# Kernel tuning notes

Measured on AMD Instinct MI355X. Metric: run time of the kernel, lower is better.

The kernel has to match this reference:

```python
import jax, jax.numpy as jnp
import numpy as np

D_MODEL = 1024
N_INPUT = 4096
N_PROCESS = 2048
D_ROUTING = 256
TEMPERATURE = 0.5
LN_EPS = 1e-5


def _gelu(x):
    return jax.nn.gelu(x, approximate=False)  # torch F.gelu default (erf)


def setup_inputs() -> dict:
    key = jax.random.key(0)
    ks = jax.random.split(key, 10)
    B, S = 8, 2048
    x = jax.random.normal(ks[0], (B, S, D_MODEL), dtype=jnp.float32)
    # GlobalRouter query_net: Linear(d_model, 2*d_routing) -> GELU -> LayerNorm -> Linear(2*d_routing, d_routing)
    W1 = jax.random.normal(ks[1], (2 * D_ROUTING, D_MODEL), dtype=jnp.float32) * (2.0 / (D_MODEL + 2 * D_ROUTING)) ** 0.5 * 1.414
    b1 = jnp.zeros((2 * D_ROUTING,), dtype=jnp.float32)
    ln_g = jnp.ones((2 * D_ROUTING,), dtype=jnp.float32)
    ln_b = jnp.zeros((2 * D_ROUTING,), dtype=jnp.float32)
    W2 = jax.random.normal(ks[2], (D_ROUTING, 2 * D_ROUTING), dtype=jnp.float32) * (2.0 / (3 * D_ROUTING)) ** 0.5 * 1.414
    b2 = jnp.zeros((D_ROUTING,), dtype=jnp.float32)
    neuron_keys = jax.random.normal(ks[3], (N_INPUT, D_ROUTING), dtype=jnp.float32) / D_ROUTING ** 0.5 * 1.414
    input_patterns = jax.random.normal(ks[4], (N_INPUT, D_MODEL), dtype=jnp.float32) / D_MODEL ** 0.5 * 1.414
    process_weights = jax.random.normal(ks[5], (N_PROCESS, N_INPUT), dtype=jnp.float32) / N_INPUT ** 0.5 * 1.414
    process_outputs = jax.random.normal(ks[6], (N_PROCESS, D_MODEL), dtype=jnp.float32) / D_MODEL ** 0.5 * 1.414
    return {
        'x': x, 'k_input': 2048, 'k_process': 1024,
        'W1': W1, 'b1': b1, 'ln_g': ln_g, 'ln_b': ln_b, 'W2': W2, 'b2': b2,
        'neuron_keys': neuron_keys, 'input_patterns': input_patterns,
        'process_weights': process_weights, 'process_outputs': process_outputs,
    }


def _forward(x, k_input, k_process, W1, b1, ln_g, ln_b, W2, b2,
             neuron_keys, input_patterns, process_weights, process_outputs):
    B, S, d_model = x.shape
    # ---- GlobalRouter ----
    gctx = jnp.max(x, axis=1)                                  # [B, d_model]
    h = _gelu(gctx @ W1.T + b1)                                # [B, 2*d_routing]
    mu = jnp.mean(h, axis=-1, keepdims=True)
    var = jnp.mean((h - mu) ** 2, axis=-1, keepdims=True)
    h = (h - mu) * jax.lax.rsqrt(var + LN_EPS) * ln_g + ln_b
    query = h @ W2.T + b2                                      # [B, d_routing]
    logits = (query @ neuron_keys.T) / D_ROUTING ** 0.5        # [B, n_input]
    probs = jax.nn.softmax(logits / TEMPERATURE, axis=-1)
    _, input_idx = jax.lax.top_k(logits, k_input)              # [B, k_input]
    one_hot = jnp.zeros_like(probs).at[jnp.arange(B)[:, None], input_idx].set(1.0)
    routing_weights = jax.lax.stop_gradient(one_hot - probs) + probs  # STE
    # ---- input neuron stage ----
    input_acts = _gelu(jnp.einsum('bsd,nd->bsn', x, input_patterns))   # [B,S,n_input]
    weighted = input_acts * routing_weights[:, None, :]
    sel_in = jnp.take_along_axis(weighted, input_idx[:, None, :], axis=2)  # [B,S,k_input]
    # gather process weight columns per batch: [B, n_process, k_input]
    W_sel = jnp.transpose(process_weights[:, input_idx], (1, 0, 2))
    process_acts = _gelu(jnp.einsum('bsk,bpk->bsp', sel_in, W_sel))    # [B,S,n_process]
    # ---- process neuron stage ----
    process_scores = jnp.mean(process_acts, axis=1)                    # [B,n_process]
    _, process_idx = jax.lax.top_k(process_scores, k_process)          # [B,k_process]
    sel_proc = jnp.take_along_axis(process_acts, process_idx[:, None, :], axis=2)  # [B,S,k_process]
    out_sel = process_outputs[process_idx]                             # [B,k_process,d_model]
    return jnp.einsum('bsp,bpd->bsd', sel_proc, out_sel)


def reference(x, k_input, k_process, W1, b1, ln_g, ln_b, W2, b2,
              neuron_keys, input_patterns, process_weights, process_outputs):
    return _forward(x, k_input, k_process, W1, b1, ln_g, ln_b, W2, b2,
                    neuron_keys, input_patterns, process_weights, process_outputs)
```

## Files before the change

### kernel.cpp

```cpp
#include <hip/hip_runtime.h>
#include <stdint.h>

#define B_  8
#define S_  2048
#define DM  1024
#define NI  4096
#define NP  2048
#define DR  256
#define H2  512
#define KI  2048
#define KP  1024
#define LDW 40

typedef __attribute__((ext_vector_type(8))) short bf16x8;
typedef __attribute__((ext_vector_type(4))) float f32x4;
typedef unsigned short ushort;
typedef unsigned int uint;

__device__ __forceinline__ float gelu_erf(float v){
    return 0.5f * v * (1.0f + erff(v * 0.7071067811865476f));
}
__device__ __forceinline__ ushort f2b(float f){
    union { float f; uint u; } a; a.f = f;
    uint r = a.u + 0x7fffu + ((a.u >> 16) & 1u);
    return (ushort)(r >> 16);
}
__device__ __forceinline__ float b2f(ushort u){
    union { uint u; float f; } a; a.u = ((uint)u) << 16; return a.f;
}
__device__ __forceinline__ void cvt8(const float* p, uint4& H, uint4& L){
    uint h[4], l[4];
    #pragma unroll
    for(int i = 0; i < 4; i++){
        ushort h0 = f2b(p[2*i]);   float f0 = b2f(h0); ushort l0 = f2b(p[2*i]   - f0);
        ushort h1 = f2b(p[2*i+1]); float f1 = b2f(h1); ushort l1 = f2b(p[2*i+1] - f1);
        h[i] = (uint)h0 | ((uint)h1 << 16);
        l[i] = (uint)l0 | ((uint)l1 << 16);
    }
    H = uint4{h[0],h[1],h[2],h[3]};
    L = uint4{l[0],l[1],l[2],l[3]};
}

__global__ __launch_bounds__(256) void k_gpart(const float* __restrict__ x,
                                               float* __restrict__ gpart){
    int b = blockIdx.x >> 4, ch = blockIdx.x & 15;
    const float4* xb = (const float4*)(x + ((size_t)b*S_ + (size_t)ch*128) * DM);
    int t = threadIdx.x;
    float4 m = xb[t];
    for(int r = 1; r < 128; r++){
        float4 v = xb[(size_t)r*(DM/4) + t];
        m.x = fmaxf(m.x, v.x); m.y = fmaxf(m.y, v.y);
        m.z = fmaxf(m.z, v.z); m.w = fmaxf(m.w, v.w);
    }
    ((float4*)(gpart + (size_t)(b*16 + ch)*DM))[t] = m;
}

__global__ __launch_bounds__(256) void k_h(const float* __restrict__ gpart,
                                           const float* __restrict__ W1,
                                           const float* __restrict__ b1,
                                           float* __restrict__ h){
    __shared__ float g[DM];
    int b = blockIdx.x >> 3, ig = blockIdx.x & 7;
    int t = threadIdx.x;
    for(int d = t; d < DM; d += 256){
        float m = gpart[(size_t)(b*16)*DM + d];
        for(int c = 1; c < 16; c++) m = fmaxf(m, gpart[(size_t)(b*16 + c)*DM + d]);
        g[d] = m;
    }
    __syncthreads();
    int i  = ig*64 + (t >> 2);
    int dq = (t & 3) * 256;
    const float* wr = W1 + (size_t)i*DM + dq;
    const float* gg = g + dq;
    float s = 0.f;
    for(int d = 0; d < 256; d++) s = fmaf(gg[d], wr[d], s);
    s += __shfl_xor(s, 1);
    s += __shfl_xor(s, 2);
    if((t & 3) == 0) h[b*H2 + i] = gelu_erf(s + b1[i]);
}

__global__ __launch_bounds__(256) void k_query(const float* __restrict__ h,
                                               const float* __restrict__ lng,
                                               const float* __restrict__ lnb,
                                               const float* __restrict__ W2,
                                               const float* __restrict__ b2,
                                               float* __restrict__ query){
    __shared__ float hn[H2];
    __shared__ float red[4];
    int b = blockIdx.x >> 2, qg = blockIdx.x & 3;
    int t = threadIdx.x;
    float v0 = h[b*H2 + t], v1 = h[b*H2 + 256 + t];
    float s = v0 + v1;
    for(int o = 32; o > 0; o >>= 1) s += __shfl_down(s, o);
    if((t & 63) == 0) red[t >> 6] = s;
    __syncthreads();
    float mean = (red[0] + red[1] + red[2] + red[3]) * (1.f/H2);
    __syncthreads();
    float d0 = v0 - mean, d1 = v1 - mean;
    float sq = d0*d0 + d1*d1;
    for(int o = 32; o > 0; o >>= 1) sq += __shfl_down(sq, o);
    if((t & 63) == 0) red[t >> 6] = sq;
    __syncthreads();
    float var  = (red[0] + red[1] + red[2] + red[3]) * (1.f/H2);
    float rstd = rsqrtf(var + 1e-5f);
    hn[t]       = d0*rstd*lng[t]       + lnb[t];
    hn[256 + t] = d1*rstd*lng[256 + t] + lnb[256 + t];
    __syncthreads();
    int q  = qg*64 + (t >> 2);
    int iq = (t & 3) * 128;
    const float* wr = W2 + (size_t)q*H2 + iq;
    float acc = 0.f;
    for(int i2 = 0; i2 < 128; i2++) acc = fmaf(hn[iq + i2], wr[i2], acc);
    acc += __shfl_xor(acc, 1);
    acc += __shfl_xor(acc, 2);
    if((t & 3) == 0) query[b*DR + q] = acc + b2[q];
}

__global__ __launch_bounds__(256) void k_logits(const float* __restrict__ query,
                                                const float* __restrict__ nk,
                                                float* __restrict__ logits){
    __shared__ float q[DR];
    int b = blockIdx.x >> 4, ng = blockIdx.x & 15;
    int t = threadIdx.x;
    if(t < DR) q[t] = query[b*DR + t];
    __syncthreads();
    int n = ng*256 + t;
    const float* kr = nk + (size_t)n*DR;
    float s = 0.f;
    for(int i = 0; i < DR; i++) s = fmaf(q[i], kr[i], s);
    logits[b*NI + n] = s * 0.0625f;
}

template<int N_, int KSEL>
__global__ __launch_bounds__(256) void k_topk(const float* __restrict__ vals,
                                              int* __restrict__ idxout){
    __shared__ unsigned u[N_];
    __shared__ int redc[4];
    __shared__ int sc[256];
    int t = threadIdx.x;
    size_t vbase = (size_t)blockIdx.x * N_;
    size_t obase = (size_t)blockIdx.x * KSEL;
    for(int i = t; i < N_; i += 256){
        unsigned bits = __float_as_uint(vals[vbase + i]);
        u[i] = (bits & 0x80000000u) ? ~bits : (bits | 0x80000000u);
    }
    __syncthreads();
    unsigned lo = 0u, hi = 0xFFFFFFFFu;
    while(lo < hi){
        unsigned mid = lo + (unsigned)((((unsigned long long)(hi - lo)) + 1ull) >> 1);
        int c = 0;
        for(int i = t; i < N_; i += 256) c += (u[i] >= mid) ? 1 : 0;
        for(int o = 32; o > 0; o >>= 1) c += __shfl_down(c, o);
        if((t & 63) == 0) redc[t >> 6] = c;
        __syncthreads();
        int tot = redc[0] + redc[1] + redc[2] + redc[3];
        if(tot >= KSEL) lo = mid; else hi = mid - 1;
        __syncthreads();
    }
    unsigned T = lo;
    const int PER = N_ / 256;
    int base = t * PER;
    int lgt = 0, leq = 0;
    for(int j = 0; j < PER; j++){
        unsigned v = u[base + j];
        lgt += (v > T) ? 1 : 0; leq += (v == T) ? 1 : 0;
    }
    sc[t] = (lgt << 16) | leq;
    __syncthreads();
    for(int o = 1; o < 256; o <<= 1){
        int add = (t >= o) ? sc[t - o] : 0;
        __syncthreads();
        sc[t] += add;
        __syncthreads();
    }
    int need = KSEL - (sc[255] >> 16);
    int ex = (t == 0) ? 0 : sc[t - 1];
    int pos = (ex >> 16) + ((ex & 0xffff) < need ? (ex & 0xffff) : need);
    int eq = ex & 0xffff;
    for(int j = 0; j < PER; j++){
        unsigned v = u[base + j];
        if(v > T){ idxout[obase + pos++] = base + j; }
        else if(v == T){ if(eq < need){ idxout[obase + pos++] = base + j; } eq++; }
    }
}

__global__ __launch_bounds__(256) void k_gemm1(const float* __restrict__ x,
                                               const float* __restrict__ patt,
                                               const int* __restrict__ iidx,
                                               ushort* __restrict__ selh,
                                               ushort* __restrict__ sell, int b0){
    __shared__ __align__(16) ushort Ah[128*LDW], Al[128*LDW], Bh[128*LDW], Bl[128*LDW];
    __shared__ int rowmap[128];
    int t = threadIdx.x;
    int g = blockIdx.x >> 8, rest = blockIdx.x & 255;
    int b = b0 + g;
    int mb = rest >> 4, nb = rest & 15;
    int m0 = mb*128, n0 = nb*128;
    ushort* selh_g = selh + (size_t)g*S_*KI;
    ushort* sell_g = sell + (size_t)g*S_*KI;
    if(t < 128) rowmap[t] = iidx[(size_t)b*KI + n0 + t];
    __syncthreads();
    int r = t & 127, half = t >> 7;
    const float* ag = x    + (size_t)b*S_*DM + (size_t)(m0 + r)*DM + half*16;
    const float* bg = patt + (size_t)rowmap[r]*DM + half*16;
    float4 fa[4], fb[4];
    #pragma unroll
    for(int i = 0; i < 4; i++){ fa[i] = *(const float4*)(ag + i*4); fb[i] = *(const float4*)(bg + i*4); }
    int w = t >> 6, lane = t & 63;
    int mbase = (w >> 1)*64, nbase = (w & 1)*64;
    int lm = lane & 15, q = lane >> 4;
    f32x4 acc[4][4];
    #pragma unroll
    for(int i = 0; i < 4; i++)
      #pragma unroll
      for(int j = 0; j < 4; j++) acc[i][j] = f32x4{0.f,0.f,0.f,0.f};
    for(int k0 = 0; k0 < DM; k0 += 32){
        uint4 AH0, AL0, AH1, AL1, BH0, BL0, BH1, BL1;
        cvt8((const float*)&fa[0], AH0, AL0); cvt8((const float*)&fa[2], AH1, AL1);
        cvt8((const float*)&fb[0], BH0, BL0); cvt8((const float*)&fb[2], BH1, BL1);
        __syncthreads();
        *(uint4*)(Ah + r*LDW + half*16)     = AH0;
        *(uint4*)(Ah + r*LDW + half*16 + 8) = AH1;
        *(uint4*)(Al + r*LDW + half*16)     = AL0;
        *(uint4*)(Al + r*LDW + half*16 + 8) = AL1;
        *(uint4*)(Bh + r*LDW + half*16)     = BH0;
        *(uint4*)(Bh + r*LDW + half*16 + 8) = BH1;
        *(uint4*)(Bl + r*LDW + half*16)     = BL0;
        *(uint4*)(Bl + r*LDW + half*16 + 8) = BL1;
        __syncthreads();
        if(k0 + 32 < DM){
            ag += 32; bg += 32;
            #pragma unroll
            for(int i = 0; i < 4; i++){ fa[i] = *(const float4*)(ag + i*4); fb[i] = *(const float4*)(bg + i*4); }
        }
        bf16x8 ahf[4], alf[4];
        #pragma unroll
        for(int mt = 0; mt < 4; mt++){
            ahf[mt] = *(const bf16x8*)(Ah + (mbase + mt*16 + lm)*LDW + q*8);
            alf[mt] = *(const bf16x8*)(Al + (mbase + mt*16 + lm)*LDW + q*8);
        }
        #pragma unroll
        for(int nt = 0; nt < 4; nt++){
            bf16x8 bhf = *(const bf16x8*)(Bh + (nbase + nt*16 + lm)*LDW + q*8);
            bf16x8 blf = *(const bf16x8*)(Bl + (nbase + nt*16 + lm)*LDW + q*8);
            #pragma unroll
            for(int mt = 0; mt < 4; mt++){
                acc[mt][nt] = __builtin_amdgcn_mfma_f32_16x16x32_bf16(ahf[mt], bhf, acc[mt][nt], 0, 0, 0);
                acc[mt][nt] = __builtin_amdgcn_mfma_f32_16x16x32_bf16(ahf[mt], blf, acc[mt][nt], 0, 0, 0);
                acc[mt][nt] = __builtin_amdgcn_mfma_f32_16x16x32_bf16(alf[mt], bhf, acc[mt][nt], 0, 0, 0);
            }
        }
    }
    #pragma unroll
    for(int mt = 0; mt < 4; mt++)
      #pragma unroll
      for(int nt = 0; nt < 4; nt++){
        int col = n0 + nbase + nt*16 + lm;
        #pragma unroll
        for(int i = 0; i < 4; i++){
            int row = m0 + mbase + mt*16 + q*4 + i;
            float gv = gelu_erf(acc[mt][nt][i]);
            ushort hbits = f2b(gv);
            selh_g[(size_t)row*KI + col] = hbits;
            sell_g[(size_t)row*KI + col] = f2b(gv - b2f(hbits));
        }
      }
}

__global__ __launch_bounds__(256) void k_gather_wsel(const float* __restrict__ pw,
                                                     const int* __restrict__ iidx,
                                                     ushort* __restrict__ wh,
                                                     ushort* __restrict__ wl,
                                                     float* __restrict__ scores, int b0){
    __shared__ int kidx[KI];
    int g = blockIdx.x >> 8, pc = blockIdx.x & 255;
    int b = b0 + g;
    ushort* wh_g = wh + (size_t)g*NP*KI;
    ushort* wl_g = wl + (size_t)g*NP*KI;
    int t = threadIdx.x;
    for(int i = t; i < KI; i += 256) kidx[i] = iidx[(size_t)b*KI + i];
    if(t < 8) scores[(size_t)b*NP + pc*8 + t] = 0.f;
    __syncthreads();
    for(int r2 = 0; r2 < 8; r2++){
        int p = pc*8 + r2;
        const float* row = pw + (size_t)p*NI;
        for(int j = t; j < KI; j += 256){
            float v = row[kidx[j]];
            ushort hb = f2b(v);
            wh_g[(size_t)p*KI + j] = hb;
            wl_g[(size_t)p*KI + j] = f2b(v - b2f(hb));
        }
    }
}

__global__ __launch_bounds__(256) void k_gemm2(const ushort* __restrict__ selh,
                                               const ushort* __restrict__ sell,
                                               const ushort* __restrict__ wh,
                                               const ushort* __restrict__ wl,
                                               ushort* __restrict__ acts,
                                               float* __restrict__ scores, int b0){
    __shared__ __align__(16) ushort Ah[128*LDW], Al[128*LDW], Bh[128*LDW], Bl[128*LDW];
    __shared__ float colsum[128];
    int t = threadIdx.x;
    int g = blockIdx.x >> 8, rest = blockIdx.x & 255;
    int b = b0 + g;
    int mb = rest >> 4, nb = rest & 15;
    int m0 = mb*128, n0 = nb*128;
    const ushort* selh_g = selh + (size_t)g*S_*KI;
    const ushort* sell_g = sell + (size_t)g*S_*KI;
    const ushort* wh_g   = wh   + (size_t)g*NP*KI;
    const ushort* wl_g   = wl   + (size_t)g*NP*KI;
    ushort* acts_g = acts + (size_t)g*S_*NP;
    int r = t & 127, half = t >> 7;
    const ushort* ahg = selh_g + (size_t)(m0 + r)*KI + half*16;
    const ushort* alg = sell_g + (size_t)(m0 + r)*KI + half*16;
    const ushort* bhg = wh_g   + (size_t)(n0 + r)*KI + half*16;
    const ushort* blg = wl_g   + (size_t)(n0 + r)*KI + half*16;
    uint4 AH0, AH1, AL0, AL1, BH0, BH1, BL0, BL1;
    AH0 = *(const uint4*)(ahg); AH1 = *(const uint4*)(ahg + 8);
    AL0 = *(const uint4*)(alg); AL1 = *(const uint4*)(alg + 8);
    BH0 = *(const uint4*)(bhg); BH1 = *(const uint4*)(bhg + 8);
    BL0 = *(const uint4*)(blg); BL1 = *(const uint4*)(blg + 8);
    int w = t >> 6, lane = t & 63;
    int mbase = (w >> 1)*64, nbase = (w & 1)*64;
    int lm = lane & 15, q = lane >> 4;
    f32x4 acc[4][4];
    #pragma unroll
    for(int i = 0; i < 4; i++)
      #pragma unroll
      for(int j = 0; j < 4; j++) acc[i][j] = f32x4{0.f,0.f,0.f,0.f};
    for(int k0 = 0; k0 < KI; k0 += 32){
        __syncthreads();
        *(uint4*)(Ah + r*LDW + half*16)     = AH0;
        *(uint4*)(Ah + r*LDW + half*16 + 8) = AH1;
        *(uint4*)(Al + r*LDW + half*16)     = AL0;
        *(uint4*)(Al + r*LDW + half*16 + 8) = AL1;
        *(uint4*)(Bh + r*LDW + half*16)     = BH0;
        *(uint4*)(Bh + r*LDW + half*16 + 8) = BH1;
        *(uint4*)(Bl + r*LDW + half*16)     = BL0;
        *(uint4*)(Bl + r*LDW + half*16 + 8) = BL1;
        __syncthreads();
        if(k0 + 32 < KI){
            ahg += 32; alg += 32; bhg += 32; blg += 32;
            AH0 = *(const uint4*)(ahg); AH1 = *(const uint4*)(ahg + 8);
            AL0 = *(const uint4*)(alg); AL1 = *(const uint4*)(alg + 8);
            BH0 = *(const uint4*)(bhg); BH1 = *(const uint4*)(bhg + 8);
            BL0 = *(const uint4*)(blg); BL1 = *(const uint4*)(blg + 8);
        }
        bf16x8 ahf[4], alf[4];
        #pragma unroll
        for(int mt = 0; mt < 4; mt++){
            ahf[mt] = *(const bf16x8*)(Ah + (mbase + mt*16 + lm)*LDW + q*8);
            alf[mt] = *(const bf16x8*)(Al + (mbase + mt*16 + lm)*LDW + q*8);
        }
        #pragma unroll
        for(int nt = 0; nt < 4; nt++){
            bf16x8 bhf = *(const bf16x8*)(Bh + (nbase + nt*16 + lm)*LDW + q*8);
            bf16x8 blf = *(const bf16x8*)(Bl + (nbase + nt*16 + lm)*LDW + q*8);
            #pragma unroll
            for(int mt = 0; mt < 4; mt++){
                acc[mt][nt] = __builtin_amdgcn_mfma_f32_16x16x32_bf16(ahf[mt], bhf, acc[mt][nt], 0, 0, 0);
                acc[mt][nt] = __builtin_amdgcn_mfma_f32_16x16x32_bf16(ahf[mt], blf, acc[mt][nt], 0, 0, 0);
                acc[mt][nt] = __builtin_amdgcn_mfma_f32_16x16x32_bf16(alf[mt], bhf, acc[mt][nt], 0, 0, 0);
            }
        }
    }
    if(t < 128) colsum[t] = 0.f;
    __syncthreads();
    #pragma unroll
    for(int mt = 0; mt < 4; mt++)
      #pragma unroll
      for(int nt = 0; nt < 4; nt++){
        int cb = nbase + nt*16 + lm;
        float s4 = 0.f;
        #pragma unroll
        for(int i = 0; i < 4; i++){
            int row = m0 + mbase + mt*16 + q*4 + i;
            float gv = gelu_erf(acc[mt][nt][i]);
            s4 += gv;
            acts_g[(size_t)row*NP + n0 + cb] = f2b(gv);
        }
        atomicAdd(&colsum[cb], s4);
      }
    __syncthreads();
    if(t < 128) atomicAdd(&scores[(size_t)b*NP + n0 + t], colsum[t]);
}

__global__ __launch_bounds__(256) void k_gather_selacts(const ushort* __restrict__ acts,
                                                        const int* __restrict__ pidx,
                                                        ushort* __restrict__ selacts, int b0){
    __shared__ int pix[KP];
    int g = blockIdx.x >> 6, sc_ = blockIdx.x & 63;
    int b = b0 + g;
    const ushort* acts_g = acts + (size_t)g*S_*NP;
    ushort* selacts_g = selacts + (size_t)g*S_*KP;
    int t = threadIdx.x;
    for(int i = t; i < KP; i += 256) pix[i] = pidx[(size_t)b*KP + i];
    __syncthreads();
    const ushort* Ab = acts_g    + ((size_t)sc_*32)*NP;
    ushort*       Ob = selacts_g + ((size_t)sc_*32)*KP;
    for(int r2 = 0; r2 < 32; r2++){
        for(int j = t; j < KP; j += 256)
            Ob[(size_t)r2*KP + j] = Ab[(size_t)r2*NP + pix[j]];
    }
}

__global__ __launch_bounds__(256) void k_gemm3(const ushort* __restrict__ selacts,
                                               const float* __restrict__ pout,
                                               const int* __restrict__ pidx,
                                               float* __restrict__ out, int b0){
    __shared__ __align__(16) ushort As[128*LDW], Bs[128*LDW];
    __shared__ int pix[KP];
    int t = threadIdx.x;
    int g = blockIdx.x >> 7, rest = blockIdx.x & 127;
    int b = b0 + g;
    int mb = rest >> 3, nb = rest & 7;
    int m0 = mb*128, n0 = nb*128;
    const ushort* selacts_g = selacts + (size_t)g*S_*KP;
    for(int i = t; i < KP; i += 256) pix[i] = pidx[(size_t)b*KP + i];
    __syncthreads();
    int r = t & 127, half = t >> 7;
    const ushort* ag = selacts_g + (size_t)(m0 + r)*KP + half*16;
    int kk = t >> 3, nc = (t & 7)*16;
    uint4 A0 = *(const uint4*)(ag), A1 = *(const uint4*)(ag + 8);
    float4 fb[4];
    {
        const float* bg = pout + (size_t)pix[kk]*DM + n0 + nc;
        #pragma unroll
        for(int i = 0; i < 4; i++) fb[i] = *(const float4*)(bg + i*4);
    }
    int w = t >> 6, lane = t & 63;
    int mbase = (w >> 1)*64, nbase = (w & 1)*64;
    int lm = lane & 15, q = lane >> 4;
    f32x4 acc[4][4];
    #pragma unroll
    for(int i = 0; i < 4; i++)
      #pragma unroll
      for(int j = 0; j < 4; j++) acc[i][j] = f32x4{0.f,0.f,0.f,0.f};
    for(int k0 = 0; k0 < KP; k0 += 32){
        __syncthreads();
        *(uint4*)(As + r*LDW + half*16)     = A0;
        *(uint4*)(As + r*LDW + half*16 + 8) = A1;
        {
            const float* pf = (const float*)fb;
            #pragma unroll
            for(int c = 0; c < 16; c++) Bs[(nc + c)*LDW + kk] = f2b(pf[c]);
        }
        __syncthreads();
        if(k0 + 32 < KP){
            ag += 32;
            A0 = *(const uint4*)(ag); A1 = *(const uint4*)(ag + 8);
            const float* bg = pout + (size_t)pix[k0 + 32 + kk]*DM + n0 + nc;
            #pragma unroll
            for(int i = 0; i < 4; i++) fb[i] = *(const float4*)(bg + i*4);
        }
        bf16x8 af[4];
        #pragma unroll
        for(int mt = 0; mt < 4; mt++)
            af[mt] = *(const bf16x8*)(As + (mbase + mt*16 + lm)*LDW + q*8);
        #pragma unroll
        for(int nt = 0; nt < 4; nt++){
            bf16x8 bf = *(const bf16x8*)(Bs + (nbase + nt*16 + lm)*LDW + q*8);
            #pragma unroll
            for(int mt = 0; mt < 4; mt++)
                acc[mt][nt] = __builtin_amdgcn_mfma_f32_16x16x32_bf16(af[mt], bf, acc[mt][nt], 0, 0, 0);
        }
    }
    float* Cb = out + (size_t)b*S_*DM;
    #pragma unroll
    for(int mt = 0; mt < 4; mt++)
      #pragma unroll
      for(int nt = 0; nt < 4; nt++){
        int col = n0 + nbase + nt*16 + lm;
        #pragma unroll
        for(int i = 0; i < 4; i++){
            int row = m0 + mbase + mt*16 + q*4 + i;
            Cb[(size_t)row*DM + col] = acc[mt][nt][i];
        }
      }
}

extern "C" void kernel_launch(void* const* d_in, const int* in_sizes, int n_in,
                              void* d_out, int out_size, void* d_ws, size_t ws_size,
                              hipStream_t stream){
    const float* x    = (const float*)d_in[0];
    const float* W1   = (const float*)d_in[3];
    const float* b1   = (const float*)d_in[4];
    const float* lng  = (const float*)d_in[5];
    const float* lnb  = (const float*)d_in[6];
    const float* W2   = (const float*)d_in[7];
    const float* b2   = (const float*)d_in[8];
    const float* nk   = (const float*)d_in[9];
    const float* patt = (const float*)d_in[10];
    const float* pw   = (const float*)d_in[11];
    const float* pout = (const float*)d_in[12];
    float* out = (float*)d_out;

    const size_t fixed =
        ((size_t)B_*16*DM*4 + 255 & ~(size_t)255) + ((size_t)B_*H2*4 + 255 & ~(size_t)255) +
        ((size_t)B_*DR*4 + 255 & ~(size_t)255)    + ((size_t)B_*NI*4 + 255 & ~(size_t)255) +
        ((size_t)B_*KI*4 + 255 & ~(size_t)255)    + ((size_t)B_*NP*4 + 255 & ~(size_t)255) +
        ((size_t)B_*KP*4 + 255 & ~(size_t)255);
    const size_t perb = (size_t)S_*KI*2*2 + (size_t)NP*KI*2*2 + (size_t)S_*NP*2 + (size_t)S_*KP*2 + 6*256;
    int G = 4;
    while(G > 1 && fixed + (size_t)G*perb > ws_size) G >>= 1;
    if(fixed + (size_t)G*perb > ws_size) return;

    char* wsp = (char*)d_ws;
    size_t off = 0;
    auto alloc = [&](size_t bytes) -> void* {
        void* p = wsp + off;
        off += (bytes + 255) & ~(size_t)255;
        return p;
    };
    float*  gpart   = (float*) alloc((size_t)B_*16*DM*4);
    float*  h       = (float*) alloc((size_t)B_*H2*4);
    float*  query   = (float*) alloc((size_t)B_*DR*4);
    float*  logits  = (float*) alloc((size_t)B_*NI*4);
    int*    iidx    = (int*)   alloc((size_t)B_*KI*4);
    float*  scores  = (float*) alloc((size_t)B_*NP*4);
    int*    pidx    = (int*)   alloc((size_t)B_*KP*4);
    ushort* selh    = (ushort*)alloc((size_t)G*S_*KI*2);
    ushort* sell    = (ushort*)alloc((size_t)G*S_*KI*2);
    ushort* wselh   = (ushort*)alloc((size_t)G*NP*KI*2);
    ushort* wsell   = (ushort*)alloc((size_t)G*NP*KI*2);
    ushort* acts    = (ushort*)alloc((size_t)G*S_*NP*2);
    ushort* selacts = (ushort*)alloc((size_t)G*S_*KP*2);

    dim3 blk(256);
    k_gpart <<<128, blk, 0, stream>>>(x, gpart);
    k_h     <<<64,  blk, 0, stream>>>(gpart, W1, b1, h);
    k_query <<<32,  blk, 0, stream>>>(h, lng, lnb, W2, b2, query);
    k_logits<<<128, blk, 0, stream>>>(query, nk, logits);
    k_topk<NI, KI><<<B_, blk, 0, stream>>>(logits, iidx);
    for(int b0 = 0; b0 < B_; b0 += G){
        k_gemm1        <<<G*256, blk, 0, stream>>>(x, patt, iidx, selh, sell, b0);
        k_gather_wsel  <<<G*256, blk, 0, stream>>>(pw, iidx, wselh, wsell, scores, b0);
        k_gemm2        <<<G*256, blk, 0, stream>>>(selh, sell, wselh, wsell, acts, scores, b0);
        k_topk<NP, KP> <<<G,     blk, 0, stream>>>(scores + (size_t)b0*NP, pidx + (size_t)b0*KP);
        k_gather_selacts<<<G*64, blk, 0, stream>>>(acts, pidx, selacts, b0);
        k_gemm3        <<<G*128, blk, 0, stream>>>(selacts, pout, pidx, out, b0);
    }
}
```

Before: 1.512 ms.

## Use fp16 MFMA for gemm1/gemm3 with pre-converted inputs and swizzled LDS

```diff
diff --git a/kernel.cpp b/kernel.cpp
--- a/kernel.cpp
+++ b/kernel.cpp
@@ -13,6 +13,7 @@
 #define LDW 40
 
 typedef __attribute__((ext_vector_type(8))) short bf16x8;
+typedef __attribute__((ext_vector_type(8))) _Float16 f16x8;
 typedef __attribute__((ext_vector_type(4))) float f32x4;
 typedef unsigned short ushort;
 typedef unsigned int uint;
@@ -28,17 +29,23 @@
 __device__ __forceinline__ float b2f(ushort u){
     union { uint u; float f; } a; a.u = ((uint)u) << 16; return a.f;
 }
-__device__ __forceinline__ void cvt8(const float* p, uint4& H, uint4& L){
-    uint h[4], l[4];
-    #pragma unroll
-    for(int i = 0; i < 4; i++){
-        ushort h0 = f2b(p[2*i]);   float f0 = b2f(h0); ushort l0 = f2b(p[2*i]   - f0);
-        ushort h1 = f2b(p[2*i+1]); float f1 = b2f(h1); ushort l1 = f2b(p[2*i+1] - f1);
-        h[i] = (uint)h0 | ((uint)h1 << 16);
-        l[i] = (uint)l0 | ((uint)l1 << 16);
-    }
-    H = uint4{h[0],h[1],h[2],h[3]};
-    L = uint4{l[0],l[1],l[2],l[3]};
+__device__ __forceinline__ ushort f2h(float f){
+    union { _Float16 h; ushort u; } v; v.h = (_Float16)f; return v.u;
+}
+
+#define SWZ_ST(r, c)  ((r)*32 + ((((c) ^ (((r) >> 1) & 3))) << 3))
+
+__global__ __launch_bounds__(256) void k_cvt(const float* __restrict__ in,
+                                             ushort* __restrict__ out, int n8){
+    int i = blockIdx.x*256 + threadIdx.x;
+    int stride = gridDim.x*256;
+    for(; i < n8; i += stride){
+        const float* p = in + (size_t)i*8;
+        ushort h[8];
+        #pragma unroll
+        for(int j = 0; j < 8; j++) h[j] = f2h(p[j]);
+        *(uint4*)(out + (size_t)i*8) = *(uint4*)h;
+    }
 }
 
 __global__ __launch_bounds__(256) void k_gpart(const float* __restrict__ x,
@@ -184,12 +191,12 @@
     }
 }
 
-__global__ __launch_bounds__(256) void k_gemm1(const float* __restrict__ x,
-                                               const float* __restrict__ patt,
+__global__ __launch_bounds__(256) void k_gemm1(const ushort* __restrict__ x16,
+                                               const ushort* __restrict__ patt16,
                                                const int* __restrict__ iidx,
                                                ushort* __restrict__ selh,
                                                ushort* __restrict__ sell, int b0){
-    __shared__ __align__(16) ushort Ah[128*LDW], Al[128*LDW], Bh[128*LDW], Bl[128*LDW];
+    __shared__ __align__(16) ushort As[128*32], Bs[128*32];
     __shared__ int rowmap[128];
     int t = threadIdx.x;
     int g = blockIdx.x >> 8, rest = blockIdx.x & 255;
@@ -200,56 +207,46 @@
     ushort* sell_g = sell + (size_t)g*S_*KI;
     if(t < 128) rowmap[t] = iidx[(size_t)b*KI + n0 + t];
     __syncthreads();
-    int r = t & 127, half = t >> 7;
-    const float* ag = x    + (size_t)b*S_*DM + (size_t)(m0 + r)*DM + half*16;
-    const float* bg = patt + (size_t)rowmap[r]*DM + half*16;
-    float4 fa[4], fb[4];
-    #pragma unroll
-    for(int i = 0; i < 4; i++){ fa[i] = *(const float4*)(ag + i*4); fb[i] = *(const float4*)(bg + i*4); }
+    int c = t & 3, r2 = t >> 2;
+    const ushort* a0p = x16 + (size_t)b*S_*DM + (size_t)(m0 + r2)*DM + c*8;
+    const ushort* a1p = a0p + (size_t)64*DM;
+    const ushort* b0p = patt16 + (size_t)rowmap[r2]*DM + c*8;
+    const ushort* b1p = patt16 + (size_t)rowmap[r2 + 64]*DM + c*8;
+    uint4 A0 = *(const uint4*)a0p, A1 = *(const uint4*)a1p;
+    uint4 B0 = *(const uint4*)b0p, B1 = *(const uint4*)b1p;
+    int st0 = SWZ_ST(r2, c);
+    int st1 = st0 + 64*32;
     int w = t >> 6, lane = t & 63;
     int mbase = (w >> 1)*64, nbase = (w & 1)*64;
     int lm = lane & 15, q = lane >> 4;
+    int fq = ((q ^ ((lm >> 1) & 3)) << 3);
     f32x4 acc[4][4];
     #pragma unroll
     for(int i = 0; i < 4; i++)
       #pragma unroll
       for(int j = 0; j < 4; j++) acc[i][j] = f32x4{0.f,0.f,0.f,0.f};
     for(int k0 = 0; k0 < DM; k0 += 32){
-        uint4 AH0, AL0, AH1, AL1, BH0, BL0, BH1, BL1;
-        cvt8((const float*)&fa[0], AH0, AL0); cvt8((const float*)&fa[2], AH1, AL1);
-        cvt8((const float*)&fb[0], BH0, BL0); cvt8((const float*)&fb[2], BH1, BL1);
-        __syncthreads();
-        *(uint4*)(Ah + r*LDW + half*16)     = AH0;
-        *(uint4*)(Ah + r*LDW + half*16 + 8) = AH1;
-        *(uint4*)(Al + r*LDW + half*16)     = AL0;
-        *(uint4*)(Al + r*LDW + half*16 + 8) = AL1;
-        *(uint4*)(Bh + r*LDW + half*16)     = BH0;
-        *(uint4*)(Bh + r*LDW + half*16 + 8) = BH1;
-        *(uint4*)(Bl + r*LDW + half*16)     = BL0;
-        *(uint4*)(Bl + r*LDW + half*16 + 8) = BL1;
+        __syncthreads();
+        *(uint4*)(As + st0) = A0; *(uint4*)(As + st1) = A1;
+        *(uint4*)(Bs + st0) = B0; *(uint4*)(Bs + st1) = B1;
         __syncthreads();
         if(k0 + 32 < DM){
-            ag += 32; bg += 32;
-            #pragma unroll
-            for(int i = 0; i < 4; i++){ fa[i] = *(const float4*)(ag + i*4); fb[i] = *(const float4*)(bg + i*4); }
-        }
-        bf16x8 ahf[4], alf[4];
-        #pragma unroll
-        for(int mt = 0; mt < 4; mt++){
-            ahf[mt] = *(const bf16x8*)(Ah + (mbase + mt*16 + lm)*LDW + q*8);
-            alf[mt] = *(const bf16x8*)(Al + (mbase + mt*16 + lm)*LDW + q*8);
-        }
-        #pragma unroll
-        for(int nt = 0; nt < 4; nt++){
-            bf16x8 bhf = *(const bf16x8*)(Bh + (nbase + nt*16 + lm)*LDW + q*8);
-            bf16x8 blf = *(const bf16x8*)(Bl + (nbase + nt*16 + lm)*LDW + q*8);
-            #pragma unroll
-            for(int mt = 0; mt < 4; mt++){
-                acc[mt][nt] = __builtin_amdgcn_mfma_f32_16x16x32_bf16(ahf[mt], bhf, acc[mt][nt], 0, 0, 0);
-                acc[mt][nt] = __builtin_amdgcn_mfma_f32_16x16x32_bf16(ahf[mt], blf, acc[mt][nt], 0, 0, 0);
-                acc[mt][nt] = __builtin_amdgcn_mfma_f32_16x16x32_bf16(alf[mt], bhf, acc[mt][nt], 0, 0, 0);
-            }
-        }
+            a0p += 32; a1p += 32; b0p += 32; b1p += 32;
+            A0 = *(const uint4*)a0p; A1 = *(const uint4*)a1p;
+            B0 = *(const uint4*)b0p; B1 = *(const uint4*)b1p;
+        }
+        f16x8 af[4], bf[4];
+        #pragma unroll
+        for(int mt = 0; mt < 4; mt++)
+            af[mt] = *(const f16x8*)(As + (mbase + mt*16 + lm)*32 + fq);
+        #pragma unroll
+        for(int nt = 0; nt < 4; nt++)
+            bf[nt] = *(const f16x8*)(Bs + (nbase + nt*16 + lm)*32 + fq);
+        #pragma unroll
+        for(int nt = 0; nt < 4; nt++)
+          #pragma unroll
+          for(int mt = 0; mt < 4; mt++)
+            acc[mt][nt] = __builtin_amdgcn_mfma_f32_16x16x32_f16(af[mt], bf[nt], acc[mt][nt], 0, 0, 0);
     }
     #pragma unroll
     for(int mt = 0; mt < 4; mt++)
@@ -299,7 +296,7 @@
                                                const ushort* __restrict__ wl,
                                                ushort* __restrict__ acts,
                                                float* __restrict__ scores, int b0){
-    __shared__ __align__(16) ushort Ah[128*LDW], Al[128*LDW], Bh[128*LDW], Bl[128*LDW];
+    __shared__ __align__(16) ushort P0[128*32], P1[128*32], P2[128*32], P3[128*32];
     __shared__ float colsum[128];
     int t = threadIdx.x;
     int g = blockIdx.x >> 8, rest = blockIdx.x & 255;
@@ -311,19 +308,21 @@
     const ushort* wh_g   = wh   + (size_t)g*NP*KI;
     const ushort* wl_g   = wl   + (size_t)g*NP*KI;
     ushort* acts_g = acts + (size_t)g*S_*NP;
-    int r = t & 127, half = t >> 7;
-    const ushort* ahg = selh_g + (size_t)(m0 + r)*KI + half*16;
-    const ushort* alg = sell_g + (size_t)(m0 + r)*KI + half*16;
-    const ushort* bhg = wh_g   + (size_t)(n0 + r)*KI + half*16;
-    const ushort* blg = wl_g   + (size_t)(n0 + r)*KI + half*16;
-    uint4 AH0, AH1, AL0, AL1, BH0, BH1, BL0, BL1;
-    AH0 = *(const uint4*)(ahg); AH1 = *(const uint4*)(ahg + 8);
-    AL0 = *(const uint4*)(alg); AL1 = *(const uint4*)(alg + 8);
-    BH0 = *(const uint4*)(bhg); BH1 = *(const uint4*)(bhg + 8);
-    BL0 = *(const uint4*)(blg); BL1 = *(const uint4*)(blg + 8);
     int w = t >> 6, lane = t & 63;
+    int c = lane & 3, r2 = lane >> 2;
+    const ushort* gp = (w == 0) ? (selh_g + (size_t)m0*KI) :
+                       (w == 1) ? (sell_g + (size_t)m0*KI) :
+                       (w == 2) ? (wh_g   + (size_t)n0*KI) :
+                                  (wl_g   + (size_t)n0*KI);
+    gp += (size_t)r2*KI + c*8;
+    ushort* Pw = (w == 0) ? P0 : (w == 1) ? P1 : (w == 2) ? P2 : P3;
+    uint4 V[8];
+    #pragma unroll
+    for(int j = 0; j < 8; j++) V[j] = *(const uint4*)(gp + (size_t)(16*j)*KI);
+    int stb = SWZ_ST(r2, c);
     int mbase = (w >> 1)*64, nbase = (w & 1)*64;
     int lm = lane & 15, q = lane >> 4;
+    int fq = ((q ^ ((lm >> 1) & 3)) << 3);
     f32x4 acc[4][4];
     #pragma unroll
     for(int i = 0; i < 4; i++)
@@ -331,32 +330,26 @@
       for(int j = 0; j < 4; j++) acc[i][j] = f32x4{0.f,0.f,0.f,0.f};
     for(int k0 = 0; k0 < KI; k0 += 32){
         __syncthreads();
-        *(uint4*)(Ah + r*LDW + half*16)     = AH0;
-        *(uint4*)(Ah + r*LDW + half*16 + 8) = AH1;
-        *(uint4*)(Al + r*LDW + half*16)     = AL0;
-        *(uint4*)(Al + r*LDW + half*16 + 8) = AL1;
-        *(uint4*)(Bh + r*LDW + half*16)     = BH0;
-        *(uint4*)(Bh + r*LDW + half*16 + 8) = BH1;
-        *(uint4*)(Bl + r*LDW + half*16)     = BL0;
-        *(uint4*)(Bl + r*LDW + half*16 + 8) = BL1;
+        #pragma unroll
+        for(int j = 0; j < 8; j++) *(uint4*)(Pw + stb + j*16*32) = V[j];
         __syncthreads();
         if(k0 + 32 < KI){
-            ahg += 32; alg += 32; bhg += 32; blg += 32;
-            AH0 = *(const uint4*)(ahg); AH1 = *(const uint4*)(ahg + 8);
-            AL0 = *(const uint4*)(alg); AL1 = *(const uint4*)(alg + 8);
-            BH0 = *(const uint4*)(bhg); BH1 = *(const uint4*)(bhg + 8);
-            BL0 = *(const uint4*)(blg); BL1 = *(const uint4*)(blg + 8);
+            gp += 32;
+            #pragma unroll
+            for(int j = 0; j < 8; j++) V[j] = *(const uint4*)(gp + (size_t)(16*j)*KI);
         }
         bf16x8 ahf[4], alf[4];
         #pragma unroll
         for(int mt = 0; mt < 4; mt++){
-            ahf[mt] = *(const bf16x8*)(Ah + (mbase + mt*16 + lm)*LDW + q*8);
-            alf[mt] = *(const bf16x8*)(Al + (mbase + mt*16 + lm)*LDW + q*8);
+            int ro = (mbase + mt*16 + lm)*32 + fq;
+            ahf[mt] = *(const bf16x8*)(P0 + ro);
+            alf[mt] = *(const bf16x8*)(P1 + ro);
         }
         #pragma unroll
         for(int nt = 0; nt < 4; nt++){
-            bf16x8 bhf = *(const bf16x8*)(Bh + (nbase + nt*16 + lm)*LDW + q*8);
-            bf16x8 blf = *(const bf16x8*)(Bl + (nbase + nt*16 + lm)*LDW + q*8);
+            int ro = (nbase + nt*16 + lm)*32 + fq;
+            bf16x8 bhf = *(const bf16x8*)(P2 + ro);
+            bf16x8 blf = *(const bf16x8*)(P3 + ro);
             #pragma unroll
             for(int mt = 0; mt < 4; mt++){
                 acc[mt][nt] = __builtin_amdgcn_mfma_f32_16x16x32_bf16(ahf[mt], bhf, acc[mt][nt], 0, 0, 0);
@@ -378,7 +371,7 @@
             int row = m0 + mbase + mt*16 + q*4 + i;
             float gv = gelu_erf(acc[mt][nt][i]);
             s4 += gv;
-            acts_g[(size_t)row*NP + n0 + cb] = f2b(gv);
+            acts_g[(size_t)row*NP + n0 + cb] = f2h(gv);
         }
         atomicAdd(&colsum[cb], s4);
       }
@@ -409,7 +402,8 @@
                                                const float* __restrict__ pout,
                                                const int* __restrict__ pidx,
                                                float* __restrict__ out, int b0){
-    __shared__ __align__(16) ushort As[128*LDW], Bs[128*LDW];
+    __shared__ __align__(16) ushort As[128*32];
+    __shared__ __align__(16) ushort Bs[128*LDW];
     __shared__ int pix[KP];
     int t = threadIdx.x;
     int g = blockIdx.x >> 7, rest = blockIdx.x & 127;
@@ -419,10 +413,13 @@
     const ushort* selacts_g = selacts + (size_t)g*S_*KP;
     for(int i = t; i < KP; i += 256) pix[i] = pidx[(size_t)b*KP + i];
     __syncthreads();
-    int r = t & 127, half = t >> 7;
-    const ushort* ag = selacts_g + (size_t)(m0 + r)*KP + half*16;
+    int c = t & 3, r2 = t >> 2;
+    const ushort* a0p = selacts_g + (size_t)(m0 + r2)*KP + c*8;
+    const ushort* a1p = a0p + (size_t)64*KP;
+    uint4 A0 = *(const uint4*)a0p, A1 = *(const uint4*)a1p;
+    int st0 = SWZ_ST(r2, c);
+    int st1 = st0 + 64*32;
     int kk = t >> 3, nc = (t & 7)*16;
-    uint4 A0 = *(const uint4*)(ag), A1 = *(const uint4*)(ag + 8);
     float4 fb[4];
     {
         const float* bg = pout + (size_t)pix[kk]*DM + n0 + nc;
@@ -432,6 +429,7 @@
     int w = t >> 6, lane = t & 63;
     int mbase = (w >> 1)*64, nbase = (w & 1)*64;
     int lm = lane & 15, q = lane >> 4;
+    int fq = ((q ^ ((lm >> 1) & 3)) << 3);
     f32x4 acc[4][4];
     #pragma unroll
     for(int i = 0; i < 4; i++)
@@ -439,31 +437,31 @@
       for(int j = 0; j < 4; j++) acc[i][j] = f32x4{0.f,0.f,0.f,0.f};
     for(int k0 = 0; k0 < KP; k0 += 32){
         __syncthreads();
-        *(uint4*)(As + r*LDW + half*16)     = A0;
-        *(uint4*)(As + r*LDW + half*16 + 8) = A1;
+        *(uint4*)(As + st0) = A0;
+        *(uint4*)(As + st1) = A1;
         {
             const float* pf = (const float*)fb;
             #pragma unroll
-            for(int c = 0; c < 16; c++) Bs[(nc + c)*LDW + kk] = f2b(pf[c]);
+            for(int c2 = 0; c2 < 16; c2++) Bs[(nc + c2)*LDW + kk] = f2h(pf[c2]);
         }
         __syncthreads();
         if(k0 + 32 < KP){
-            ag += 32;
-            A0 = *(const uint4*)(ag); A1 = *(const uint4*)(ag + 8);
+            a0p += 32; a1p += 32;
+            A0 = *(const uint4*)a0p; A1 = *(const uint4*)a1p;
             const float* bg = pout + (size_t)pix[k0 + 32 + kk]*DM + n0 + nc;
             #pragma unroll
             for(int i = 0; i < 4; i++) fb[i] = *(const float4*)(bg + i*4);
         }
-        bf16x8 af[4];
+        f16x8 af[4];
         #pragma unroll
         for(int mt = 0; mt < 4; mt++)
-            af[mt] = *(const bf16x8*)(As + (mbase + mt*16 + lm)*LDW + q*8);
+            af[mt] = *(const f16x8*)(As + (mbase + mt*16 + lm)*32 + fq);
         #pragma unroll
         for(int nt = 0; nt < 4; nt++){
-            bf16x8 bf = *(const bf16x8*)(Bs + (nbase + nt*16 + lm)*LDW + q*8);
+            f16x8 bf = *(const f16x8*)(Bs + (nbase + nt*16 + lm)*LDW + q*8);
             #pragma unroll
             for(int mt = 0; mt < 4; mt++)
-                acc[mt][nt] = __builtin_amdgcn_mfma_f32_16x16x32_bf16(af[mt], bf, acc[mt][nt], 0, 0, 0);
+                acc[mt][nt] = __builtin_amdgcn_mfma_f32_16x16x32_f16(af[mt], bf, acc[mt][nt], 0, 0, 0);
         }
     }
     float* Cb = out + (size_t)b*S_*DM;
@@ -496,12 +494,15 @@
     const float* pout = (const float*)d_in[12];
     float* out = (float*)d_out;
 
-    const size_t fixed =
-        ((size_t)B_*16*DM*4 + 255 & ~(size_t)255) + ((size_t)B_*H2*4 + 255 & ~(size_t)255) +
-        ((size_t)B_*DR*4 + 255 & ~(size_t)255)    + ((size_t)B_*NI*4 + 255 & ~(size_t)255) +
-        ((size_t)B_*KI*4 + 255 & ~(size_t)255)    + ((size_t)B_*NP*4 + 255 & ~(size_t)255) +
-        ((size_t)B_*KP*4 + 255 & ~(size_t)255);
-    const size_t perb = (size_t)S_*KI*2*2 + (size_t)NP*KI*2*2 + (size_t)S_*NP*2 + (size_t)S_*KP*2 + 6*256;
+    const size_t A256 = 255;
+    auto rnd = [&](size_t v){ return (v + A256) & ~A256; };
+    const size_t fixed = rnd((size_t)B_*16*DM*4) + rnd((size_t)B_*H2*4) +
+                         rnd((size_t)B_*DR*4) + rnd((size_t)B_*NI*4) +
+                         rnd((size_t)B_*KI*4) + rnd((size_t)B_*NP*4) +
+                         rnd((size_t)B_*KP*4) +
+                         rnd((size_t)B_*S_*DM*2) + rnd((size_t)NI*DM*2);
+    const size_t perb = rnd((size_t)S_*KI*2) * 2 + rnd((size_t)NP*KI*2) * 2 +
+                        rnd((size_t)S_*NP*2) + rnd((size_t)S_*KP*2);
     int G = 4;
     while(G > 1 && fixed + (size_t)G*perb > ws_size) G >>= 1;
     if(fixed + (size_t)G*perb > ws_size) return;
@@ -510,7 +511,7 @@
     size_t off = 0;
     auto alloc = [&](size_t bytes) -> void* {
         void* p = wsp + off;
-        off += (bytes + 255) & ~(size_t)255;
+        off += rnd(bytes);
         return p;
     };
     float*  gpart   = (float*) alloc((size_t)B_*16*DM*4);
@@ -520,6 +521,8 @@
     int*    iidx    = (int*)   alloc((size_t)B_*KI*4);
     float*  scores  = (float*) alloc((size_t)B_*NP*4);
     int*    pidx    = (int*)   alloc((size_t)B_*KP*4);
+    ushort* x16     = (ushort*)alloc((size_t)B_*S_*DM*2);
+    ushort* patt16  = (ushort*)alloc((size_t)NI*DM*2);
     ushort* selh    = (ushort*)alloc((size_t)G*S_*KI*2);
     ushort* sell    = (ushort*)alloc((size_t)G*S_*KI*2);
     ushort* wselh   = (ushort*)alloc((size_t)G*NP*KI*2);
@@ -528,13 +531,15 @@
     ushort* selacts = (ushort*)alloc((size_t)G*S_*KP*2);
 
     dim3 blk(256);
+    k_cvt   <<<2048, blk, 0, stream>>>(x, x16, (int)((size_t)B_*S_*DM/8));
+    k_cvt   <<<1024, blk, 0, stream>>>(patt, patt16, (int)((size_t)NI*DM/8));
     k_gpart <<<128, blk, 0, stream>>>(x, gpart);
     k_h     <<<64,  blk, 0, stream>>>(gpart, W1, b1, h);
     k_query <<<32,  blk, 0, stream>>>(h, lng, lnb, W2, b2, query);
     k_logits<<<128, blk, 0, stream>>>(query, nk, logits);
     k_topk<NI, KI><<<B_, blk, 0, stream>>>(logits, iidx);
     for(int b0 = 0; b0 < B_; b0 += G){
-        k_gemm1        <<<G*256, blk, 0, stream>>>(x, patt, iidx, selh, sell, b0);
+        k_gemm1        <<<G*256, blk, 0, stream>>>(x16, patt16, iidx, selh, sell, b0);
         k_gather_wsel  <<<G*256, blk, 0, stream>>>(pw, iidx, wselh, wsell, scores, b0);
         k_gemm2        <<<G*256, blk, 0, stream>>>(selh, sell, wselh, wsell, acts, scores, b0);
         k_topk<NP, KP> <<<G,     blk, 0, stream>>>(scores + (size_t)b0*NP, pidx + (size_t)b0*KP);
```

New measurement: 2.474 ms. 1.64x slower.
